# Kernel optimization log

Hardware: AMD Instinct MI355X
Metric: run time of the kernel (lower is better)

Reference implementation:

```python
import jax, jax.numpy as jnp
import numpy as np

EPS = 1e-7

# Poincare ball, curvature c = 1 (hyparticle-net default manifold)

def _mobius_add(x, y):
    x2 = jnp.sum(x * x, axis=-1, keepdims=True)
    y2 = jnp.sum(y * y, axis=-1, keepdims=True)
    xy = jnp.sum(x * y, axis=-1, keepdims=True)
    num = (1.0 + 2.0 * xy + y2) * x + (1.0 - x2) * y
    den = 1.0 + 2.0 * xy + x2 * y2
    return num / jnp.maximum(den, EPS)


def _lambda_x(x):
    # conformal factor lambda_x = 2 / (1 - ||x||^2)
    return 2.0 / jnp.clip(1.0 - jnp.sum(x * x, axis=-1, keepdims=True), EPS, None)


def _logmap(y, x):
    # log map of y at base point x
    u = _mobius_add(-x, y)
    un = jnp.clip(jnp.linalg.norm(u, axis=-1, keepdims=True), EPS, 1.0 - 1e-5)
    return (2.0 / _lambda_x(x)) * jnp.arctanh(un) * (u / un)


def _expmap(v, x):
    # exp map of tangent vector v at base point x
    vn = jnp.clip(jnp.linalg.norm(v, axis=-1, keepdims=True), EPS, None)
    second = jnp.tanh(_lambda_x(x) * vn * 0.5) * (v / vn)
    return _mobius_add(x, second)


def setup_inputs() -> dict:
    key = jax.random.key(0)
    k1, k2 = jax.random.split(key)
    N, D = 1024, 64
    u = jax.random.normal(k1, (N, D), dtype=jnp.float32)
    # points strictly inside the unit ball (norm < 0.5)
    x = 0.5 * u / (1.0 + jnp.linalg.norm(u, axis=-1, keepdims=True))
    adj = jax.random.randint(k2, (N, N), 0, 2, dtype=jnp.int32)
    return {"x": x, "adj": adj}


def reference(x, adj):
    mask = adj > 0                                   # [N, N]
    # all-pairs logmap: logs[i, j] = log_{x_i}(x_j)   [N, N, D]
    logs = jax.vmap(lambda xi: _logmap(x, xi))(x)
    v = jnp.sum(jnp.where(mask[..., None], logs, 0.0), axis=1)  # [N, D]
    return _expmap(v, x)                             # [N, D]
```

## Files before the change

kernel.cpp:

```cpp
#include <hip/hip_runtime.h>

#define EPSF 1e-7f

__device__ __forceinline__ float rcp_fast(float x) { return __builtin_amdgcn_rcpf(x); }

__device__ __forceinline__ int swz(int r, int c) { return r * 16 + (c ^ ((r >> 2) & 7)); }

__device__ __forceinline__ float dot4(float4 v) {
    return v.x * v.x + v.y * v.y + v.z * v.z + v.w * v.w;
}

__global__ __launch_bounds__(256, 2) void pair_kernel(
    const float* __restrict__ x, const int* __restrict__ adj,
    float* __restrict__ T, float* __restrict__ alphaPart) {
    const int N = 1024;
    const int j0 = blockIdx.x * 64;
    const int i0 = blockIdx.y * 32;
    const int t = threadIdx.x;
    const int h = t & 1;
    const int q = t >> 1;
    const int qx = q & 15;
    const int qy = q >> 4;

    __shared__ float4 ti4[32 * 16];
    __shared__ float4 tj4[64 * 16];
    __shared__ float x2i_l[32];
    __shared__ float y2_l[64];

    const float4* x4 = reinterpret_cast<const float4*>(x);
#pragma unroll
    for (int k = 0; k < 2; ++k) {
        const int f = k * 256 + t;
        const int r = f >> 4, c = f & 15;
        float4 v = x4[(size_t)i0 * 16 + f];
        ti4[swz(r, c)] = v;
        float s = dot4(v);
#pragma unroll
        for (int off = 1; off <= 8; off <<= 1) s += __shfl_xor(s, off, 64);
        if ((t & 15) == 0) x2i_l[r] = s;
    }
#pragma unroll
    for (int k = 0; k < 4; ++k) {
        const int f = k * 256 + t;
        const int r = f >> 4, c = f & 15;
        float4 v = x4[(size_t)j0 * 16 + f];
        tj4[swz(r, c)] = v;
        float s = dot4(v);
#pragma unroll
        for (int off = 1; off <= 8; off <<= 1) s += __shfl_xor(s, off, 64);
        if ((t & 15) == 0) y2_l[r] = s;
    }
    __syncthreads();

    float acc[4][4];
#pragma unroll
    for (int a = 0; a < 4; ++a)
#pragma unroll
        for (int b = 0; b < 4; ++b) acc[a][b] = 0.f;

#pragma unroll
    for (int cc = 0; cc < 8; ++cc) {
        const int c = h * 8 + cc;
        float4 xiv[4], xjv[4];
#pragma unroll
        for (int a = 0; a < 4; ++a) xiv[a] = ti4[swz(qy * 4 + a, c)];
#pragma unroll
        for (int b = 0; b < 4; ++b) xjv[b] = tj4[swz(qx * 4 + b, c)];
#pragma unroll
        for (int a = 0; a < 4; ++a)
#pragma unroll
            for (int b = 0; b < 4; ++b) {
                acc[a][b] = fmaf(xiv[a].x, xjv[b].x, acc[a][b]);
                acc[a][b] = fmaf(xiv[a].y, xjv[b].y, acc[a][b]);
                acc[a][b] = fmaf(xiv[a].z, xjv[b].z, acc[a][b]);
                acc[a][b] = fmaf(xiv[a].w, xjv[b].w, acc[a][b]);
            }
    }
#pragma unroll
    for (int a = 0; a < 4; ++a)
#pragma unroll
        for (int b = 0; b < 4; ++b) acc[a][b] += __shfl_xor(acc[a][b], 1, 64);

    const int ib = i0 + qy * 4;
    const int jb = j0 + qx * 4;
    const int bsel = h * 2;
    const float y2[2] = {y2_l[qx * 4 + bsel], y2_l[qx * 4 + bsel + 1]};

    float svsum[4];
#pragma unroll
    for (int a = 0; a < 4; ++a) {
        const int2 aj = *reinterpret_cast<const int2*>(&adj[(size_t)(ib + a) * N + jb + bsel]);
        const int m[2] = {aj.x, aj.y};
        const float x2a = x2i_l[qy * 4 + a];
        const float onemx2 = 1.f - x2a;
        const float onemx2c = fmaxf(onemx2, EPSF);
        float tv2[2];
        float ssum = 0.f;
#pragma unroll
        for (int bb = 0; bb < 2; ++bb) {
            const float dot = acc[a][bsel + bb];
            const float c1 = fmaf(-2.f, dot, 1.f);
            const float A = c1 + y2[bb];
            const float den = fmaxf(fmaf(x2a, y2[bb], c1), EPSF);
            const float rd = rcp_fast(den);
            const float av = -A * rd;
            const float bv = onemx2 * rd;
            float un2 = av * av * x2a;
            un2 = fmaf(bv * bv, y2[bb], un2);
            un2 = fmaf(2.f * av * bv, dot, un2);
            un2 = fmaxf(un2, 0.f);
            float un = sqrtf(un2);
            un = fminf(fmaxf(un, EPSF), 1.0f - 1e-5f);
            const float ratio = (1.f + un) * rcp_fast(1.f - un);
            const float at = 0.34657359027997264f * __log2f(ratio);
            const float g = onemx2c * at * rcp_fast(un);
            const float sv = m[bb] ? g * av : 0.f;
            const float tv = m[bb] ? g * bv : 0.f;
            ssum += sv;
            tv2[bb] = tv;
        }
        float2 tw = {tv2[0], tv2[1]};
        *reinterpret_cast<float2*>(&T[(size_t)(ib + a) * N + jb + bsel]) = tw;
        svsum[a] = ssum;
    }

#pragma unroll
    for (int off = 1; off <= 16; off <<= 1) {
#pragma unroll
        for (int a = 0; a < 4; ++a) svsum[a] += __shfl_xor(svsum[a], off, 64);
    }
    if ((t & 31) == 0) {
#pragma unroll
        for (int a = 0; a < 4; ++a)
            alphaPart[(size_t)blockIdx.x * N + ib + a] = svsum[a];
    }
}

__global__ __launch_bounds__(512, 2) void out_kernel(
    const float* __restrict__ x, const float* __restrict__ T,
    const float* __restrict__ alphaPart, float* __restrict__ out) {
    const int N = 1024, D = 64;
    const int i0 = blockIdx.x * 4;
    const int w = threadIdx.x >> 6;
    const int d = threadIdx.x & 63;
    const int jw = __builtin_amdgcn_readfirstlane(w * 128);

    const float4* T0 = reinterpret_cast<const float4*>(T + (size_t)(i0 + 0) * N + jw);
    const float4* T1 = reinterpret_cast<const float4*>(T + (size_t)(i0 + 1) * N + jw);
    const float4* T2 = reinterpret_cast<const float4*>(T + (size_t)(i0 + 2) * N + jw);
    const float4* T3 = reinterpret_cast<const float4*>(T + (size_t)(i0 + 3) * N + jw);
    const float* xbase = x + (size_t)jw * D + d;

    float acc[4][4];
#pragma unroll
    for (int r = 0; r < 4; ++r)
#pragma unroll
        for (int c = 0; c < 4; ++c) acc[r][c] = 0.f;

#pragma unroll 4
    for (int q = 0; q < 32; ++q) {
        const float4 tq[4] = {T0[q], T1[q], T2[q], T3[q]};
        const float* xp = xbase + (size_t)q * 4 * D;
        const float x0 = xp[0 * D], x1 = xp[1 * D], x2v = xp[2 * D], x3 = xp[3 * D];
#pragma unroll
        for (int r = 0; r < 4; ++r) {
            acc[r][0] = fmaf(tq[r].x, x0, acc[r][0]);
            acc[r][1] = fmaf(tq[r].y, x1, acc[r][1]);
            acc[r][2] = fmaf(tq[r].z, x2v, acc[r][2]);
            acc[r][3] = fmaf(tq[r].w, x3, acc[r][3]);
        }
    }

    __shared__ float part[4][8][64];
#pragma unroll
    for (int r = 0; r < 4; ++r)
        part[r][w][d] = (acc[r][0] + acc[r][1]) + (acc[r][2] + acc[r][3]);
    __syncthreads();

    if (threadIdx.x < 256) {
        const int r = threadIdx.x >> 6;
        const int i = i0 + r;
        float v = 0.f;
#pragma unroll
        for (int ww = 0; ww < 8; ++ww) v += part[r][ww][d];

        float ap = (d < 16) ? alphaPart[(size_t)d * N + i] : 0.f;
#pragma unroll
        for (int off = 1; off < 64; off <<= 1) ap += __shfl_xor(ap, off, 64);

        const float xid = x[(size_t)i * D + d];
        float x2i = xid * xid;
#pragma unroll
        for (int off = 1; off < 64; off <<= 1) x2i += __shfl_xor(x2i, off, 64);
        const float onemx2 = 1.f - x2i;
        const float onemx2c = fmaxf(onemx2, EPSF);
        v = fmaf(ap, xid, v);

        float vn2 = v * v;
#pragma unroll
        for (int off = 1; off < 64; off <<= 1) vn2 += __shfl_xor(vn2, off, 64);
        const float vn = fmaxf(sqrtf(vn2), EPSF);
        const float arg = vn * rcp_fast(onemx2c);
        const float th = tanhf(arg);
        const float sec = th * rcp_fast(vn) * v;

        float xy = xid * sec;
        float y2p = sec * sec;
#pragma unroll
        for (int off = 1; off < 64; off <<= 1) {
            xy += __shfl_xor(xy, off, 64);
            y2p += __shfl_xor(y2p, off, 64);
        }
        const float numd = (1.f + 2.f * xy + y2p) * xid + onemx2 * sec;
        const float den2 = fmaxf(fmaf(x2i, y2p, 1.f + 2.f * xy), EPSF);
        out[(size_t)i * D + d] = numd * rcp_fast(den2);
    }
}

extern "C" void kernel_launch(void* const* d_in, const int* in_sizes, int n_in,
                              void* d_out, int out_size, void* d_ws, size_t ws_size,
                              hipStream_t stream) {
    const float* x = (const float*)d_in[0];
    const int* adj = (const int*)d_in[1];
    float* out = (float*)d_out;
    const int N = 1024;

    float* T = (float*)d_ws;
    float* alphaPart = (float*)((char*)d_ws + (size_t)N * N * 4);

    hipLaunchKernelGGL(pair_kernel, dim3(16, 32), dim3(256), 0, stream, x, adj, T, alphaPart);
    hipLaunchKernelGGL(out_kernel, dim3(N / 4), dim3(512), 0, stream, x, T, alphaPart, out);
}
```

Baseline: 20.39 us.

## Double threads per block in both kernels, splitting dot and j-range further

The pair kernel now uses 512 threads, with four lanes splitting each 4x4 dot-product tile over the D dimension. Each lane then handles one column of the elementwise hyperbolic math instead of two, which means one scalar adj load and one T store per element. The out kernel uses 1024 threads, so each wave covers 64 j values instead of 128 and the partial-sum reduction grows to 16 entries. The aim is more parallelism and shorter per-thread serial work. The cost is extra shuffle reductions, narrower memory accesses, and heavier cross-wave reduction.

```diff
diff --git a/kernel.cpp b/kernel.cpp
--- a/kernel.cpp
+++ b/kernel.cpp
@@ -10,15 +10,15 @@
     return v.x * v.x + v.y * v.y + v.z * v.z + v.w * v.w;
 }
 
-__global__ __launch_bounds__(256, 2) void pair_kernel(
+__global__ __launch_bounds__(512, 4) void pair_kernel(
     const float* __restrict__ x, const int* __restrict__ adj,
     float* __restrict__ T, float* __restrict__ alphaPart) {
     const int N = 1024;
     const int j0 = blockIdx.x * 64;
     const int i0 = blockIdx.y * 32;
     const int t = threadIdx.x;
-    const int h = t & 1;
-    const int q = t >> 1;
+    const int h2 = t & 3;
+    const int q = t >> 2;
     const int qx = q & 15;
     const int qy = q >> 4;
 
@@ -28,11 +28,9 @@
     __shared__ float y2_l[64];
 
     const float4* x4 = reinterpret_cast<const float4*>(x);
-#pragma unroll
-    for (int k = 0; k < 2; ++k) {
-        const int f = k * 256 + t;
-        const int r = f >> 4, c = f & 15;
-        float4 v = x4[(size_t)i0 * 16 + f];
+    {
+        const int r = t >> 4, c = t & 15;
+        float4 v = x4[(size_t)i0 * 16 + t];
         ti4[swz(r, c)] = v;
         float s = dot4(v);
 #pragma unroll
@@ -40,8 +38,8 @@
         if ((t & 15) == 0) x2i_l[r] = s;
     }
 #pragma unroll
-    for (int k = 0; k < 4; ++k) {
-        const int f = k * 256 + t;
+    for (int k = 0; k < 2; ++k) {
+        const int f = k * 512 + t;
         const int r = f >> 4, c = f & 15;
         float4 v = x4[(size_t)j0 * 16 + f];
         tj4[swz(r, c)] = v;
@@ -59,8 +57,8 @@
         for (int b = 0; b < 4; ++b) acc[a][b] = 0.f;
 
 #pragma unroll
-    for (int cc = 0; cc < 8; ++cc) {
-        const int c = h * 8 + cc;
+    for (int cc = 0; cc < 4; ++cc) {
+        const int c = h2 * 4 + cc;
         float4 xiv[4], xjv[4];
 #pragma unroll
         for (int a = 0; a < 4; ++a) xiv[a] = ti4[swz(qy * 4 + a, c)];
@@ -79,71 +77,65 @@
 #pragma unroll
     for (int a = 0; a < 4; ++a)
 #pragma unroll
-        for (int b = 0; b < 4; ++b) acc[a][b] += __shfl_xor(acc[a][b], 1, 64);
+        for (int b = 0; b < 4; ++b) {
+            acc[a][b] += __shfl_xor(acc[a][b], 1, 64);
+            acc[a][b] += __shfl_xor(acc[a][b], 2, 64);
+        }
 
     const int ib = i0 + qy * 4;
     const int jb = j0 + qx * 4;
-    const int bsel = h * 2;
-    const float y2[2] = {y2_l[qx * 4 + bsel], y2_l[qx * 4 + bsel + 1]};
+    const int jcol = jb + h2;
+    const float y2c = y2_l[qx * 4 + h2];
 
     float svsum[4];
 #pragma unroll
     for (int a = 0; a < 4; ++a) {
-        const int2 aj = *reinterpret_cast<const int2*>(&adj[(size_t)(ib + a) * N + jb + bsel]);
-        const int m[2] = {aj.x, aj.y};
+        const int m = adj[(size_t)(ib + a) * N + jcol];
         const float x2a = x2i_l[qy * 4 + a];
         const float onemx2 = 1.f - x2a;
         const float onemx2c = fmaxf(onemx2, EPSF);
-        float tv2[2];
-        float ssum = 0.f;
-#pragma unroll
-        for (int bb = 0; bb < 2; ++bb) {
-            const float dot = acc[a][bsel + bb];
-            const float c1 = fmaf(-2.f, dot, 1.f);
-            const float A = c1 + y2[bb];
-            const float den = fmaxf(fmaf(x2a, y2[bb], c1), EPSF);
-            const float rd = rcp_fast(den);
-            const float av = -A * rd;
-            const float bv = onemx2 * rd;
-            float un2 = av * av * x2a;
-            un2 = fmaf(bv * bv, y2[bb], un2);
-            un2 = fmaf(2.f * av * bv, dot, un2);
-            un2 = fmaxf(un2, 0.f);
-            float un = sqrtf(un2);
-            un = fminf(fmaxf(un, EPSF), 1.0f - 1e-5f);
-            const float ratio = (1.f + un) * rcp_fast(1.f - un);
-            const float at = 0.34657359027997264f * __log2f(ratio);
-            const float g = onemx2c * at * rcp_fast(un);
-            const float sv = m[bb] ? g * av : 0.f;
-            const float tv = m[bb] ? g * bv : 0.f;
-            ssum += sv;
-            tv2[bb] = tv;
-        }
-        float2 tw = {tv2[0], tv2[1]};
-        *reinterpret_cast<float2*>(&T[(size_t)(ib + a) * N + jb + bsel]) = tw;
-        svsum[a] = ssum;
-    }
-
-#pragma unroll
-    for (int off = 1; off <= 16; off <<= 1) {
+        const float dot = acc[a][h2];
+        const float c1 = fmaf(-2.f, dot, 1.f);
+        const float A = c1 + y2c;
+        const float den = fmaxf(fmaf(x2a, y2c, c1), EPSF);
+        const float rd = rcp_fast(den);
+        const float av = -A * rd;
+        const float bv = onemx2 * rd;
+        float un2 = av * av * x2a;
+        un2 = fmaf(bv * bv, y2c, un2);
+        un2 = fmaf(2.f * av * bv, dot, un2);
+        un2 = fmaxf(un2, 0.f);
+        float un = sqrtf(un2);
+        un = fminf(fmaxf(un, EPSF), 1.0f - 1e-5f);
+        const float ratio = (1.f + un) * rcp_fast(1.f - un);
+        const float at = 0.34657359027997264f * __log2f(ratio);
+        const float g = onemx2c * at * rcp_fast(un);
+        const float sv = m ? g * av : 0.f;
+        const float tv = m ? g * bv : 0.f;
+        T[(size_t)(ib + a) * N + jcol] = tv;
+        svsum[a] = sv;
+    }
+
+#pragma unroll
+    for (int off = 1; off < 64; off <<= 1) {
 #pragma unroll
         for (int a = 0; a < 4; ++a) svsum[a] += __shfl_xor(svsum[a], off, 64);
     }
-    if ((t & 31) == 0) {
+    if ((t & 63) == 0) {
 #pragma unroll
         for (int a = 0; a < 4; ++a)
             alphaPart[(size_t)blockIdx.x * N + ib + a] = svsum[a];
     }
 }
 
-__global__ __launch_bounds__(512, 2) void out_kernel(
+__global__ __launch_bounds__(1024, 4) void out_kernel(
     const float* __restrict__ x, const float* __restrict__ T,
     const float* __restrict__ alphaPart, float* __restrict__ out) {
     const int N = 1024, D = 64;
     const int i0 = blockIdx.x * 4;
     const int w = threadIdx.x >> 6;
     const int d = threadIdx.x & 63;
-    const int jw = __builtin_amdgcn_readfirstlane(w * 128);
+    const int jw = __builtin_amdgcn_readfirstlane(w * 64);
 
     const float4* T0 = reinterpret_cast<const float4*>(T + (size_t)(i0 + 0) * N + jw);
     const float4* T1 = reinterpret_cast<const float4*>(T + (size_t)(i0 + 1) * N + jw);
@@ -158,7 +150,7 @@
         for (int c = 0; c < 4; ++c) acc[r][c] = 0.f;
 
 #pragma unroll 4
-    for (int q = 0; q < 32; ++q) {
+    for (int q = 0; q < 16; ++q) {
         const float4 tq[4] = {T0[q], T1[q], T2[q], T3[q]};
         const float* xp = xbase + (size_t)q * 4 * D;
         const float x0 = xp[0 * D], x1 = xp[1 * D], x2v = xp[2 * D], x3 = xp[3 * D];
@@ -171,7 +163,7 @@
         }
     }
 
-    __shared__ float part[4][8][64];
+    __shared__ float part[4][16][64];
 #pragma unroll
     for (int r = 0; r < 4; ++r)
         part[r][w][d] = (acc[r][0] + acc[r][1]) + (acc[r][2] + acc[r][3]);
@@ -182,7 +174,7 @@
         const int i = i0 + r;
         float v = 0.f;
 #pragma unroll
-        for (int ww = 0; ww < 8; ++ww) v += part[r][ww][d];
+        for (int ww = 0; ww < 16; ++ww) v += part[r][ww][d];
 
         float ap = (d < 16) ? alphaPart[(size_t)d * N + i] : 0.f;
 #pragma unroll
@@ -228,6 +220,6 @@
     float* T = (float*)d_ws;
     float* alphaPart = (float*)((char*)d_ws + (size_t)N * N * 4);
 
-    hipLaunchKernelGGL(pair_kernel, dim3(16, 32), dim3(256), 0, stream, x, adj, T, alphaPart);
-    hipLaunchKernelGGL(out_kernel, dim3(N / 4), dim3(512), 0, stream, x, T, alphaPart, out);
-}
+    hipLaunchKernelGGL(pair_kernel, dim3(16, 32), dim3(512), 0, stream, x, adj, T, alphaPart);
+    hipLaunchKernelGGL(out_kernel, dim3(N / 4), dim3(1024), 0, stream, x, T, alphaPart, out);
+}
```

New measurement: 19.54 us, median of 2. -4.2%, faster.
